# Kernel optimization log

Measured on AMD Instinct MI355X. Metric: run time of the kernel, lower is better.

The kernel has to match this reference:

```python
import math
import jax, jax.numpy as jnp
import numpy as np

SCALES = [0.25, 1.0]


def _window_lengths(N):
    Ls = []
    for s in SCALES:
        Ls.append(int(math.floor(N * math.sqrt(s))))
        Ls.append(int(math.floor(N / math.sqrt(s))))
    return Ls


def _extract_windows(feature_seq, L):
    """feature_seq: (B, C, N) -> (B, N, C, L) windows centered at each position,
    zero-padded where the window extends outside [0, N)."""
    B, C, N = feature_seq.shape
    half = L // 2
    # idx[center, j] = center - half + j
    idx = jnp.arange(N)[:, None] - half + jnp.arange(L)[None, :]  # (N, L)
    valid = (idx >= 0) & (idx < N)
    gathered = feature_seq[:, :, jnp.clip(idx, 0, N - 1)]  # (B, C, N, L)
    gathered = jnp.where(valid[None, None, :, :], gathered, jnp.zeros((), feature_seq.dtype))
    return jnp.transpose(gathered, (0, 2, 1, 3))  # (B, N, C, L)


def setup_inputs() -> dict:
    key = jax.random.key(0)
    feature_seq = jax.random.normal(key, (2, 64, 512), dtype=jnp.float32)
    return {"feature_seq": feature_seq}


def reference(feature_seq):
    B, C, N = feature_seq.shape
    return tuple(_extract_windows(feature_seq, L) for L in _window_lengths(N))
```

## Files before the change

kernel.cpp:

```cpp
#include <hip/hip_runtime.h>

constexpr int B = 2;
constexpr int C = 64;
constexpr int N = 512;

template <int L>
__global__ __launch_bounds__(256)
void win_kernel(const float* __restrict__ in, float* __restrict__ out) {
    constexpr int HALF = L / 2;
    constexpr int L4 = L / 4;
    constexpr int L4_BITS = (L == 256) ? 6 : (L == 512) ? 7 : 8;

    int t = blockIdx.x * blockDim.x + threadIdx.x;

    int l4 = t & (L4 - 1);
    int rest = t >> L4_BITS;
    int c = rest & (C - 1);
    rest >>= 6;
    int n = rest & (N - 1);
    int b = rest >> 9;

    const float* __restrict__ row = in + (b * C + c) * N;
    int idx = n - HALF + (l4 << 2);

    float4 v;
    v.x = ((unsigned)(idx)     < (unsigned)N) ? row[idx]     : 0.0f;
    v.y = ((unsigned)(idx + 1) < (unsigned)N) ? row[idx + 1] : 0.0f;
    v.z = ((unsigned)(idx + 2) < (unsigned)N) ? row[idx + 2] : 0.0f;
    v.w = ((unsigned)(idx + 3) < (unsigned)N) ? row[idx + 3] : 0.0f;

    reinterpret_cast<float4*>(out)[t] = v;
}

extern "C" void kernel_launch(void* const* d_in, const int* in_sizes, int n_in,
                              void* d_out, int out_size, void* d_ws, size_t ws_size,
                              hipStream_t stream) {
    const float* in = (const float*)d_in[0];
    float* out = (float*)d_out;

    constexpr long long SZ256  = (long long)B * N * C * 256;
    constexpr long long SZ1024 = (long long)B * N * C * 1024;
    constexpr long long SZ512  = (long long)B * N * C * 512;

    float* out0 = out;
    float* out1 = out0 + SZ256;
    float* out2 = out1 + SZ1024;
    float* out3 = out2 + SZ512;

    constexpr int THREADS = 256;
    constexpr int G256  = (int)(SZ256  / 4 / THREADS);
    constexpr int G1024 = (int)(SZ1024 / 4 / THREADS);
    constexpr int G512  = (int)(SZ512  / 4 / THREADS);

    win_kernel<256> <<<G256,  THREADS, 0, stream>>>(in, out0);
    win_kernel<1024><<<G1024, THREADS, 0, stream>>>(in, out1);
    win_kernel<512> <<<G512,  THREADS, 0, stream>>>(in, out2);
    win_kernel<512> <<<G512,  THREADS, 0, stream>>>(in, out3);
}
```

Baseline: 126.3 us.

## Fuse four window kernels into one launch with nontemporal vector stores

Replaces four separate kernel launches with a single kernel that dispatches on block index to the right window length and output segment. Each thread now writes four float4 outputs in an unrolled loop, and stores use nontemporal hints to avoid polluting cache with the large write-only output. This targets inter-launch gaps and tail effects, as well as cache pressure from streaming stores. It adds branch dispatch per block and fewer total blocks.

```diff
diff --git a/kernel.cpp b/kernel.cpp
--- a/kernel.cpp
+++ b/kernel.cpp
@@ -1,35 +1,71 @@
 #include <hip/hip_runtime.h>
+
 
 constexpr int B = 2;
 constexpr int C = 64;
 constexpr int N = 512;
 
+constexpr int SZ256  = B * N * C * 256;
+constexpr int SZ1024 = B * N * C * 1024;
+constexpr int SZ512  = B * N * C * 512;
+
+constexpr int BLK256  = SZ256  / 4 / 1024;
+constexpr int BLK1024 = SZ1024 / 4 / 1024;
+constexpr int BLK512  = SZ512  / 4 / 1024;
+constexpr int NBLK = BLK256 + BLK1024 + 2 * BLK512;
+
+typedef float f32x4 __attribute__((ext_vector_type(4)));
+
 template <int L>
-__global__ __launch_bounds__(256)
-void win_kernel(const float* __restrict__ in, float* __restrict__ out) {
+__device__ __forceinline__ void do_seg(const float* __restrict__ in,
+                                       float* __restrict__ out,
+                                       int blk, int tid) {
     constexpr int HALF = L / 2;
     constexpr int L4 = L / 4;
     constexpr int L4_BITS = (L == 256) ? 6 : (L == 512) ? 7 : 8;
 
-    int t = blockIdx.x * blockDim.x + threadIdx.x;
+    const int base = blk * 1024;
+    f32x4* __restrict__ out4 = reinterpret_cast<f32x4*>(out);
 
-    int l4 = t & (L4 - 1);
-    int rest = t >> L4_BITS;
-    int c = rest & (C - 1);
-    rest >>= 6;
-    int n = rest & (N - 1);
-    int b = rest >> 9;
+#pragma unroll
+    for (int k = 0; k < 4; ++k) {
+        int t = base + k * 256 + tid;
 
-    const float* __restrict__ row = in + (b * C + c) * N;
-    int idx = n - HALF + (l4 << 2);
+        int l4 = t & (L4 - 1);
+        int rest = t >> L4_BITS;
+        int c = rest & (C - 1);
+        rest >>= 6;
+        int n = rest & (N - 1);
+        int b = rest >> 9;
 
-    float4 v;
-    v.x = ((unsigned)(idx)     < (unsigned)N) ? row[idx]     : 0.0f;
-    v.y = ((unsigned)(idx + 1) < (unsigned)N) ? row[idx + 1] : 0.0f;
-    v.z = ((unsigned)(idx + 2) < (unsigned)N) ? row[idx + 2] : 0.0f;
-    v.w = ((unsigned)(idx + 3) < (unsigned)N) ? row[idx + 3] : 0.0f;
+        const float* __restrict__ row = in + (b * C + c) * N;
+        int idx = n - HALF + (l4 << 2);
 
-    reinterpret_cast<float4*>(out)[t] = v;
+        f32x4 v;
+        v.x = ((unsigned)(idx)     < (unsigned)N) ? row[idx]     : 0.0f;
+        v.y = ((unsigned)(idx + 1) < (unsigned)N) ? row[idx + 1] : 0.0f;
+        v.z = ((unsigned)(idx + 2) < (unsigned)N) ? row[idx + 2] : 0.0f;
+        v.w = ((unsigned)(idx + 3) < (unsigned)N) ? row[idx + 3] : 0.0f;
+
+        __builtin_nontemporal_store(v, out4 + t);
+    }
+}
+
+__global__ __launch_bounds__(256)
+void msw_fused_kernel(const float* __restrict__ in, float* __restrict__ out) {
+    const int blk = blockIdx.x;
+    const int tid = threadIdx.x;
+
+    if (blk < BLK256) {
+        do_seg<256>(in, out, blk, tid);
+    } else if (blk < BLK256 + BLK1024) {
+        do_seg<1024>(in, out + SZ256, blk - BLK256, tid);
+    } else if (blk < BLK256 + BLK1024 + BLK512) {
+        do_seg<512>(in, out + SZ256 + SZ1024, blk - (BLK256 + BLK1024), tid);
+    } else {
+        do_seg<512>(in, out + SZ256 + SZ1024 + SZ512,
+                    blk - (BLK256 + BLK1024 + BLK512), tid);
+    }
 }
 
 extern "C" void kernel_launch(void* const* d_in, const int* in_sizes, int n_in,
@@ -38,22 +74,5 @@
     const float* in = (const float*)d_in[0];
     float* out = (float*)d_out;
 
-    constexpr long long SZ256  = (long long)B * N * C * 256;
-    constexpr long long SZ1024 = (long long)B * N * C * 1024;
-    constexpr long long SZ512  = (long long)B * N * C * 512;
-
-    float* out0 = out;
-    float* out1 = out0 + SZ256;
-    float* out2 = out1 + SZ1024;
-    float* out3 = out2 + SZ512;
-
-    constexpr int THREADS = 256;
-    constexpr int G256  = (int)(SZ256  / 4 / THREADS);
-    constexpr int G1024 = (int)(SZ1024 / 4 / THREADS);
-    constexpr int G512  = (int)(SZ512  / 4 / THREADS);
-
-    win_kernel<256> <<<G256,  THREADS, 0, stream>>>(in, out0);
-    win_kernel<1024><<<G1024, THREADS, 0, stream>>>(in, out1);
-    win_kernel<512> <<<G512,  THREADS, 0, stream>>>(in, out2);
-    win_kernel<512> <<<G512,  THREADS, 0, stream>>>(in, out3);
+    msw_fused_kernel<<<NBLK, 256, 0, stream>>>(in, out);
 }
```

Measured after the change: 123.5 us. 1.02x faster.
